# Kernel tuning notes

Measured on AMD Instinct MI355X. Metric: run time of the kernel, lower is better.

The kernel has to match this reference:

```python
import jax, jax.numpy as jnp
import numpy as np

D_IN, D_HIDDEN, DT_RANK, D_MEM, STEP = 256, 64, 16, 128, 16
B_, L_ = 2, 2048
S = 0.02  # weight init scale

def generate_a(d_in, d_hidden):
    i = jnp.arange(d_in, dtype=jnp.float32)[:, None]
    j = jnp.arange(d_hidden, dtype=jnp.float32)[None, :]
    off = jnp.sqrt(2.0 * i + 1.0) * jnp.sqrt(2.0 * j + 1.0)
    return jnp.where(i == j, i + 1.0, jnp.where(i > j, off, 0.0))

def setup_inputs():
    key = jax.random.key(0)
    ks = jax.random.split(key, 10)
    d_out = 3 * D_HIDDEN + 2 * D_IN + 2 * DT_RANK
    return {
        "x": jax.random.normal(ks[0], (B_, L_, D_IN), jnp.float32),
        "W_xproj": jax.random.normal(ks[1], (D_IN, d_out), jnp.float32) * S,
        "W_dt": jax.random.normal(ks[2], (DT_RANK, D_IN), jnp.float32) * S,
        "b_dt": jnp.full((D_IN,), -11.0, jnp.float32),
        "W_dtl": jax.random.normal(ks[3], (DT_RANK, D_IN), jnp.float32) * S,
        "b_dtl": jnp.full((D_IN,), -11.0, jnp.float32),
        "A": generate_a(D_IN, D_HIDDEN),
        "Dp": jnp.ones((D_IN,), jnp.float32),
        "W_Q": jax.random.normal(ks[4], (D_IN, D_MEM), jnp.float32) * S,
        "b_Q": jnp.zeros((D_MEM,), jnp.float32),
        "W_K": jax.random.normal(ks[5], (D_IN, D_MEM), jnp.float32) * S,
        "b_K": jnp.zeros((D_MEM,), jnp.float32),
        "W_V": jax.random.normal(ks[6], (D_IN, D_MEM), jnp.float32) * S,
        "b_V": jnp.zeros((D_MEM,), jnp.float32),
        "W_O": jax.random.normal(ks[7], (D_MEM, D_IN), jnp.float32) * S,
        "b_O": jnp.zeros((D_IN,), jnp.float32),
    }

def _selective_scan(u, delta, A, Bm, Cm, Dp):
    # u, delta: (b,l,d); A: (d,n); Bm, Cm: (b,l,n)
    dA = jnp.exp(jnp.einsum('bld,dn->bldn', delta, A))          # (b,l,d,n)
    dBu = delta[..., None] * Bm[:, :, None, :] * u[..., None]   # (b,l,d,n)
    def comb(e1, e2):
        a1, b1 = e1
        a2, b2 = e2
        return a2 * a1, a2 * b1 + b2
    _, xs = jax.lax.associative_scan(comb, (dA, dBu), axis=1)   # states (b,l,d,n)
    y = jnp.einsum('bldn,bln->bld', xs, Cm)
    if Dp is not None:
        y = y + u * Dp
    return y

def reference(x, W_xproj, W_dt, b_dt, W_dtl, b_dtl, A, Dp, W_Q, b_Q, W_K, b_K, W_V, b_V, W_O, b_O):
    proj = x @ W_xproj  # (b,l,3n+2d+2r)
    splits = np.cumsum([D_HIDDEN, D_HIDDEN, D_HIDDEN, D_IN, D_IN, DT_RANK]).tolist()
    Bm, Bl, Cm, E, Fg, dt, dtl = jnp.split(proj, splits, axis=-1)
    delta = jax.nn.softplus(dt @ W_dt + b_dt)       # delta_softplus=True folded in
    delta_l = jax.nn.softplus(dtl @ W_dtl + b_dtl)
    y = _selective_scan(x, delta, A, Bm, Cm, Dp)
    y_local = _selective_scan(x, delta_l, A, Bl, jnp.ones_like(Bl), None)  # C=ones, D=None
    memory = y_local[:, ::STEP, :]                  # strided checkpoints (b,m,d)
    Q = x @ W_Q + b_Q
    K = memory @ W_K + b_K
    V = memory @ W_V + b_V
    # note: original scales by sqrt(d_hidden), not sqrt(d_memory)
    w = jax.nn.softmax(jnp.einsum('blm,bkm->blk', Q, K) / jnp.sqrt(jnp.float32(D_HIDDEN)), axis=-1)
    att = jnp.einsum('blk,bkm->blm', w, V) @ W_O + b_O
    return y + att * E + x * Fg
```

## Files before the change

### kernel.cpp

```cpp
#include <hip/hip_runtime.h>
#include <math.h>

#define D_INN 256
#define D_HID 64
#define DTR 16
#define D_MEMM 128
#define BB 2
#define LL 2048
#define NROWS (BB*LL)
#define NPROJ 736
#define NTOT 864
#define SEG 16
#define SEGLEN (LL/SEG)
#define NCHUNK (LL/8)

typedef __attribute__((ext_vector_type(8))) short short8v;
typedef __attribute__((ext_vector_type(4))) float float4v;

static __device__ __forceinline__ unsigned short f2bf(float f) {
    unsigned int u = __float_as_uint(f);
    u += 0x7fff + ((u >> 16) & 1);
    return (unsigned short)(u >> 16);
}

static __device__ __forceinline__ float rdlane(float v, int l) {
    return __uint_as_float(__builtin_amdgcn_readlane(__float_as_uint(v), l));
}

#define PK(g, b, chunk, n, li) (((((size_t)(g)*BB + (b)) * NCHUNK + (chunk)) * 64 + (n)) * 8 + (li))

__global__ __launch_bounds__(256) void k_gemm(const float* __restrict__ x,
        const float* __restrict__ Wx, const float* __restrict__ Wq,
        const float* __restrict__ bq, float* __restrict__ proj,
        float* __restrict__ packed) {
    __shared__ unsigned short As[64][40];
    __shared__ unsigned short Bs[64][40];
    const int t = threadIdx.x;
    const int lane = t & 63, w = t >> 6;
    const int wr = w >> 1, wc = w & 1;
    const int row0 = blockIdx.y * 64, col0 = blockIdx.x * 64;

    float4v acc[2][2];
    #pragma unroll
    for (int i = 0; i < 2; i++)
        #pragma unroll
        for (int j = 0; j < 2; j++) acc[i][j] = (float4v)0.f;

    const int ar = t >> 2, akq = (t & 3) * 8;
    const int bk = t >> 3, bcq = (t & 7) * 8;

    for (int k0 = 0; k0 < D_INN; k0 += 32) {
        float4 a0 = *(const float4*)&x[(size_t)(row0 + ar) * D_INN + k0 + akq];
        float4 a1 = *(const float4*)&x[(size_t)(row0 + ar) * D_INN + k0 + akq + 4];
        float4 b0 = {}, b1 = {};
        int col = col0 + bcq;
        if (col + 8 <= NPROJ) {
            b0 = *(const float4*)&Wx[(size_t)(k0 + bk) * NPROJ + col];
            b1 = *(const float4*)&Wx[(size_t)(k0 + bk) * NPROJ + col + 4];
        } else if (col < NTOT) {
            b0 = *(const float4*)&Wq[(size_t)(k0 + bk) * D_MEMM + (col - NPROJ)];
            b1 = *(const float4*)&Wq[(size_t)(k0 + bk) * D_MEMM + (col - NPROJ) + 4];
        }
        __syncthreads();
        {
            unsigned short av[8] = { f2bf(a0.x), f2bf(a0.y), f2bf(a0.z), f2bf(a0.w),
                                     f2bf(a1.x), f2bf(a1.y), f2bf(a1.z), f2bf(a1.w) };
            *(short8v*)&As[ar][akq] = *(short8v*)av;
            Bs[bcq + 0][bk] = f2bf(b0.x); Bs[bcq + 1][bk] = f2bf(b0.y);
            Bs[bcq + 2][bk] = f2bf(b0.z); Bs[bcq + 3][bk] = f2bf(b0.w);
            Bs[bcq + 4][bk] = f2bf(b1.x); Bs[bcq + 5][bk] = f2bf(b1.y);
            Bs[bcq + 6][bk] = f2bf(b1.z); Bs[bcq + 7][bk] = f2bf(b1.w);
        }
        __syncthreads();
        short8v af[2], bf[2];
        const int fr = lane & 15, fk = (lane >> 4) * 8;
        af[0] = *(short8v*)&As[wr * 32 + fr][fk];
        af[1] = *(short8v*)&As[wr * 32 + 16 + fr][fk];
        bf[0] = *(short8v*)&Bs[wc * 32 + fr][fk];
        bf[1] = *(short8v*)&Bs[wc * 32 + 16 + fr][fk];
        #pragma unroll
        for (int i = 0; i < 2; i++)
            #pragma unroll
            for (int j = 0; j < 2; j++)
                acc[i][j] = __builtin_amdgcn_mfma_f32_16x16x32_bf16(af[i], bf[j], acc[i][j], 0, 0, 0);
    }
    #pragma unroll
    for (int i = 0; i < 2; i++)
        #pragma unroll
        for (int j = 0; j < 2; j++) {
            int cc = col0 + wc * 32 + j * 16 + (lane & 15);
            int rr0 = row0 + wr * 32 + i * 16 + (lane >> 4) * 4;
            if (cc < 192) {
                int g = cc >> 6, n = cc & 63;
                int bb = rr0 >> 11, l = rr0 & (LL - 1);
                float4 pk = make_float4(acc[i][j][0], acc[i][j][1], acc[i][j][2], acc[i][j][3]);
                *(float4*)&packed[PK(g, bb, l >> 3, n, l & 7)] = pk;
            } else {
                #pragma unroll
                for (int e = 0; e < 4; e++) {
                    float v = acc[i][j][e];
                    if (cc >= NPROJ) v += bq[cc - NPROJ];
                    proj[(size_t)(rr0 + e) * NTOT + cc] = v;
                }
            }
        }
}

__global__ __launch_bounds__(256) void k_xt(const float* __restrict__ x,
        float* __restrict__ xT) {
    __shared__ float tile[64][65];
    const int t = threadIdx.x;
    const int lt = blockIdx.x * 64, dt = blockIdx.y * 64, b = blockIdx.z;
    const int c = t & 63, rg = (t >> 6) * 16;
    #pragma unroll
    for (int j = 0; j < 16; ++j)
        tile[rg + j][c] = x[((size_t)b * LL + lt + rg + j) * D_INN + dt + c];
    __syncthreads();
    #pragma unroll
    for (int j = 0; j < 16; ++j)
        xT[((size_t)b * D_INN + dt + rg + j) * LL + lt + c] = tile[c][rg + j];
}

__global__ __launch_bounds__(256) void k_delta(const float* __restrict__ proj,
        const float* __restrict__ Wdt, const float* __restrict__ bdt,
        const float* __restrict__ Wdtl, const float* __restrict__ bdtl,
        float* __restrict__ deltaT, float* __restrict__ deltalT) {
    __shared__ float sdt[16][17], sdtl[16][17];
    const int t = threadIdx.x;
    const int r0 = blockIdx.x * 16;
    const int b = r0 >> 11, l0 = r0 & (LL - 1);
    {
        int r = t >> 4, c = t & 15;
        sdt[r][c]  = proj[(size_t)(r0 + r) * NTOT + 704 + c];
        sdtl[r][c] = proj[(size_t)(r0 + r) * NTOT + 720 + c];
    }
    __syncthreads();
    float w1[DTR], w2[DTR];
    #pragma unroll
    for (int r = 0; r < DTR; r++) {
        w1[r] = Wdt[r * D_INN + t];
        w2[r] = Wdtl[r * D_INN + t];
    }
    const float b1 = bdt[t], b2 = bdtl[t];
    float o1[16], o2[16];
    #pragma unroll
    for (int row = 0; row < 16; ++row) {
        float a1 = b1, a2 = b2;
        #pragma unroll
        for (int r = 0; r < DTR; r++) {
            a1 += sdt[row][r] * w1[r];
            a2 += sdtl[row][r] * w2[r];
        }
        o1[row] = (a1 > 20.f) ? a1 : log1pf(expf(a1));
        o2[row] = (a2 > 20.f) ? a2 : log1pf(expf(a2));
    }
    float* p1 = &deltaT[((size_t)b * D_INN + t) * LL + l0];
    float* p2 = &deltalT[((size_t)b * D_INN + t) * LL + l0];
    #pragma unroll
    for (int j = 0; j < 16; j += 4) {
        *(float4*)&p1[j] = make_float4(o1[j], o1[j+1], o1[j+2], o1[j+3]);
        *(float4*)&p2[j] = make_float4(o2[j], o2[j+1], o2[j+2], o2[j+3]);
    }
}

template<int SCAN>
__global__ __launch_bounds__(256) void k_scan1t(const float* __restrict__ xT,
        const float* __restrict__ packed, const float* __restrict__ A,
        const float* __restrict__ dTall,
        float* __restrict__ Qbuf, float* __restrict__ SDbuf,
        float* __restrict__ cumd, float* __restrict__ mem) {
    const int t = threadIdx.x;
    const int w = t >> 6, n = t & 63;
    const int b = blockIdx.y, seg = blockIdx.z;
    const int d = blockIdx.x * 4 + w;
    const float* dT = dTall + ((size_t)b * D_INN + d) * LL + seg * SEGLEN;
    const float* uT = xT + ((size_t)b * D_INN + d) * LL + seg * SEGLEN;
    const float Aln = A[d * D_HID + n] * 1.44269504f;
    const int lr = n & 7;
    const float* Bp = packed + PK(SCAN, b, seg * 16, 0, 0);

    float s = 0.f, sd = 0.f;
    for (int c = 0; c < 16; ++c) {
        float dvl = dT[c * 8 + lr];
        float pl  = dvl * uT[c * 8 + lr];
        float4 B0 = *(const float4*)&Bp[((size_t)c * 64 + n) * 8];
        float4 B1 = *(const float4*)&Bp[((size_t)c * 64 + n) * 8 + 4];
        float Bv[8] = {B0.x, B0.y, B0.z, B0.w, B1.x, B1.y, B1.z, B1.w};
        {
            float dv = rdlane(dvl, 0), p = rdlane(pl, 0);
            s = fmaf(exp2f(dv * Aln), s, p * Bv[0]);
            sd += dv;
        }
        if (SCAN == 1 && (c & 1) == 0) {
            float v = s;
            #pragma unroll
            for (int off = 32; off >= 1; off >>= 1) v += __shfl_xor(v, off);
            if (n == 0) {
                int k = seg * 8 + (c >> 1);
                mem[((size_t)b * 128 + k) * D_INN + d] = v;
                cumd[(((size_t)b * SEG + seg) * 8 + (c >> 1)) * D_INN + d] = sd;
            }
        }
        #pragma unroll
        for (int li = 1; li < 8; ++li) {
            float dv = rdlane(dvl, li), p = rdlane(pl, li);
            s = fmaf(exp2f(dv * Aln), s, p * Bv[li]);
            sd += dv;
        }
    }
    Qbuf[((((size_t)SCAN * 2 + b) * SEG + seg) * D_INN + d) * 64 + n] = s;
    if (n == 0) SDbuf[(((size_t)SCAN * 2 + b) * SEG + seg) * D_INN + d] = sd;
}

__global__ __launch_bounds__(256) void k_scan2(const float* __restrict__ xT,
        const float* __restrict__ packed, const float* __restrict__ A,
        const float* __restrict__ Dp, const float* __restrict__ deltaT,
        const float* __restrict__ Qbuf, const float* __restrict__ SDbuf,
        float* __restrict__ y) {
    __shared__ float rbuf[4][8][65];
    const int t = threadIdx.x;
    const int w = t >> 6, n = t & 63;
    const int b = blockIdx.y, seg = blockIdx.z;
    const int d = blockIdx.x * 4 + w;
    const size_t rowbase = (size_t)b * LL + (size_t)seg * SEGLEN;
    const float* dT = deltaT + ((size_t)b * D_INN + d) * LL + seg * SEGLEN;
    const float* uT = xT + ((size_t)b * D_INN + d) * LL + seg * SEGLEN;
    const float Aln = A[d * D_HID + n] * 1.44269504f;
    const float Dpv = Dp[d];
    const int lr = n & 7;
    const int rli = n >> 3, g = n & 7;
    const float* Bp = packed + PK(0, b, seg * 16, 0, 0);
    const float* Cp = packed + PK(2, b, seg * 16, 0, 0);

    float s = 0.f;
    for (int k = 0; k < seg; ++k) {
        float sdk = SDbuf[(((size_t)b * SEG + k) * D_INN + d)];
        float Qk = Qbuf[(((size_t)b * SEG + k) * D_INN + d) * 64 + n];
        s = fmaf(exp2f(sdk * Aln), s, Qk);
    }

    for (int c = 0; c < 16; ++c) {
        const size_t l0 = rowbase + c * 8;
        float dvl = dT[c * 8 + lr];
        float uvl = uT[c * 8 + lr];
        float pl = dvl * uvl;
        float4 B0 = *(const float4*)&Bp[((size_t)c * 64 + n) * 8];
        float4 B1 = *(const float4*)&Bp[((size_t)c * 64 + n) * 8 + 4];
        float4 C0 = *(const float4*)&Cp[((size_t)c * 64 + n) * 8];
        float4 C1 = *(const float4*)&Cp[((size_t)c * 64 + n) * 8 + 4];
        float Bv[8] = {B0.x, B0.y, B0.z, B0.w, B1.x, B1.y, B1.z, B1.w};
        float Cv[8] = {C0.x, C0.y, C0.z, C0.w, C1.x, C1.y, C1.z, C1.w};
        #pragma unroll
        for (int li = 0; li < 8; ++li) {
            float dv = rdlane(dvl, li);
            float p  = rdlane(pl, li);
            s = fmaf(exp2f(dv * Aln), s, p * Bv[li]);
            rbuf[w][li][n] = s * Cv[li];
        }
        float acc = 0.f;
        #pragma unroll
        for (int j = 0; j < 8; ++j) acc += rbuf[w][rli][g * 8 + j];
        acc += __shfl_xor(acc, 1);
        acc += __shfl_xor(acc, 2);
        acc += __shfl_xor(acc, 4);
        float uv = __shfl(uvl, rli);
        if (g == 0) {
            y[(l0 + rli) * D_INN + d] = acc + uv * Dpv;
        }
    }
}

__global__ __launch_bounds__(256) void k_sin(const float* __restrict__ A,
        const float* __restrict__ Qbuf, const float* __restrict__ SDbuf,
        float* __restrict__ Sin) {
    const int t = threadIdx.x, w = t >> 6, n = t & 63;
    const int b = blockIdx.y;
    const int d = blockIdx.x * 4 + w;
    const float Aln = A[d * D_HID + n] * 1.44269504f;
    float s = 0.f;
    #pragma unroll
    for (int seg = 0; seg < SEG; ++seg) {
        if (seg > 0) Sin[(((size_t)b * SEG + seg) * D_INN + d) * 64 + n] = s;
        float sdk = SDbuf[((size_t)(2 + b) * SEG + seg) * D_INN + d];
        float Qk = Qbuf[(((size_t)(2 + b) * SEG + seg) * D_INN + d) * 64 + n];
        s = fmaf(exp2f(sdk * Aln), s, Qk);
    }
}

__global__ __launch_bounds__(256) void k_fix(const float* __restrict__ A,
        const float* __restrict__ Sin, const float* __restrict__ cumd,
        float* __restrict__ mem) {
    const int t = threadIdx.x, w = t >> 6, n = t & 63;
    const int k = 8 + blockIdx.y;
    const int b = blockIdx.z;
    const int d = blockIdx.x * 4 + w;
    const int seg = k >> 3;
    const float Aln = A[d * D_HID + n] * 1.44269504f;
    float cum = cumd[((size_t)b * 128 + k) * D_INN + d];
    float sv = Sin[(((size_t)b * SEG + seg) * D_INN + d) * 64 + n];
    float v = exp2f(cum * Aln) * sv;
    #pragma unroll
    for (int off = 32; off >= 1; off >>= 1) v += __shfl_xor(v, off);
    if (n == 0) mem[((size_t)b * 128 + k) * D_INN + d] += v;
}

__global__ __launch_bounds__(128) void k_kvwo(const float* __restrict__ mem,
        const float* __restrict__ Wk, const float* __restrict__ bk,
        const float* __restrict__ Wv, const float* __restrict__ bv,
        const float* __restrict__ Wo,
        float* __restrict__ K, float* __restrict__ VWo) {
    __shared__ float mrow[256];
    __shared__ float vrow[128];
    const int k = blockIdx.x, b = blockIdx.y;
    const int t = threadIdx.x;
    const float* mr = mem + ((size_t)b * 128 + k) * D_INN;
    mrow[t] = mr[t];
    mrow[t + 128] = mr[t + 128];
    __syncthreads();
    float aK = bk[t], aV = bv[t];
    for (int dd = 0; dd < D_INN; dd++) {
        float m = mrow[dd];
        aK += m * Wk[dd * D_MEMM + t];
        aV += m * Wv[dd * D_MEMM + t];
    }
    K[((size_t)b * 128 + k) * D_MEMM + t] = aK;
    vrow[t] = aV;
    __syncthreads();
    float a0 = 0.f, a1 = 0.f;
    for (int m = 0; m < 128; ++m) {
        float vm = vrow[m];
        a0 += vm * Wo[(size_t)m * D_INN + t];
        a1 += vm * Wo[(size_t)m * D_INN + t + 128];
    }
    VWo[((size_t)b * 128 + k) * D_INN + t] = a0;
    VWo[((size_t)b * 128 + k) * D_INN + t + 128] = a1;
}

__global__ __launch_bounds__(256) void k_attn(const float* __restrict__ x,
        const float* __restrict__ proj, const float* __restrict__ y,
        const float* __restrict__ K, const float* __restrict__ VWo,
        const float* __restrict__ bo, float* __restrict__ out) {
    __shared__ float qs[16][132];
    __shared__ float ws[16][132];
    __shared__ float denom[16];
    const int t = threadIdx.x;
    const int b = blockIdx.y;
    const int r0 = blockIdx.x * 16;
    const size_t rowbase = (size_t)b * LL + r0;
    {
        int r = t >> 4, c8 = (t & 15) * 8;
        const float* src = &proj[(rowbase + r) * NTOT + NPROJ + c8];
        *(float4*)&qs[r][c8] = *(const float4*)src;
        *(float4*)&qs[r][c8 + 4] = *(const float4*)(src + 4);
    }
    __syncthreads();
    {
        const int k = t & 127, rg = (t >> 7) * 8;
        const float* Kr = K + ((size_t)b * 128 + k) * D_MEMM;
        float acc[8] = {};
        #pragma unroll 8
        for (int m = 0; m < 128; m += 4) {
            float4 kv = *(const float4*)&Kr[m];
            #pragma unroll
            for (int r = 0; r < 8; ++r) {
                float4 qv = *(const float4*)&qs[rg + r][m];
                acc[r] += qv.x * kv.x + qv.y * kv.y + qv.z * kv.z + qv.w * kv.w;
            }
        }
        #pragma unroll
        for (int r = 0; r < 8; ++r) ws[rg + r][k] = acc[r] * 0.125f;
    }
    __syncthreads();
    {
        const int r = t >> 4, j = t & 15;
        float4 v0 = *(float4*)&ws[r][j * 8];
        float4 v1 = *(float4*)&ws[r][j * 8 + 4];
        float mx = fmaxf(fmaxf(fmaxf(v0.x, v0.y), fmaxf(v0.z, v0.w)),
                         fmaxf(fmaxf(v1.x, v1.y), fmaxf(v1.z, v1.w)));
        #pragma unroll
        for (int o = 1; o < 16; o <<= 1) mx = fmaxf(mx, __shfl_xor(mx, o));
        v0.x = expf(v0.x - mx); v0.y = expf(v0.y - mx);
        v0.z = expf(v0.z - mx); v0.w = expf(v0.w - mx);
        v1.x = expf(v1.x - mx); v1.y = expf(v1.y - mx);
        v1.z = expf(v1.z - mx); v1.w = expf(v1.w - mx);
        float sum = v0.x + v0.y + v0.z + v0.w + v1.x + v1.y + v1.z + v1.w;
        #pragma unroll
        for (int o = 1; o < 16; o <<= 1) sum += __shfl_xor(sum, o);
        *(float4*)&ws[r][j * 8] = v0;
        *(float4*)&ws[r][j * 8 + 4] = v1;
        if (j == 0) denom[r] = sum;
    }
    __syncthreads();
    {
        const int w = t >> 6, lane = t & 63;
        const int c0 = lane * 4;
        const float* vb = VWo + (size_t)b * 128 * D_INN + c0;
        float acc[4][4] = {};
        #pragma unroll 8
        for (int k = 0; k < 128; k += 4) {
            float4 wv[4];
            #pragma unroll
            for (int r = 0; r < 4; ++r) wv[r] = *(float4*)&ws[w * 4 + r][k];
            #pragma unroll
            for (int kk = 0; kk < 4; ++kk) {
                float4 vw = *(const float4*)&vb[(size_t)(k + kk) * D_INN];
                #pragma unroll
                for (int r = 0; r < 4; ++r) {
                    float wk = (kk == 0 ? wv[r].x : kk == 1 ? wv[r].y : kk == 2 ? wv[r].z : wv[r].w);
                    acc[r][0] += wk * vw.x; acc[r][1] += wk * vw.y;
                    acc[r][2] += wk * vw.z; acc[r][3] += wk * vw.w;
                }
            }
        }
        float4 bov = *(const float4*)&bo[c0];
        #pragma unroll
        for (int r = 0; r < 4; ++r) {
            size_t rr = rowbase + w * 4 + r;
            float dn = 1.f / denom[w * 4 + r];
            float4 yv = *(const float4*)&y[rr * D_INN + c0];
            float4 xv = *(const float4*)&x[rr * D_INN + c0];
            float4 Ev = *(const float4*)&proj[rr * NTOT + 192 + c0];
            float4 Fv = *(const float4*)&proj[rr * NTOT + 448 + c0];
            float4 o;
            o.x = yv.x + (acc[r][0] * dn + bov.x) * Ev.x + xv.x * Fv.x;
            o.y = yv.y + (acc[r][1] * dn + bov.y) * Ev.y + xv.y * Fv.y;
            o.z = yv.z + (acc[r][2] * dn + bov.z) * Ev.z + xv.z * Fv.z;
            o.w = yv.w + (acc[r][3] * dn + bov.w) * Ev.w + xv.w * Fv.w;
            *(float4*)&out[rr * D_INN + c0] = o;
        }
    }
}

extern "C" void kernel_launch(void* const* d_in, const int* in_sizes, int n_in,
                              void* d_out, int out_size, void* d_ws, size_t ws_size,
                              hipStream_t stream) {
    const float* x    = (const float*)d_in[0];
    const float* Wx   = (const float*)d_in[1];
    const float* Wdt  = (const float*)d_in[2];
    const float* bdt  = (const float*)d_in[3];
    const float* Wdtl = (const float*)d_in[4];
    const float* bdtl = (const float*)d_in[5];
    const float* A    = (const float*)d_in[6];
    const float* Dp   = (const float*)d_in[7];
    const float* Wq   = (const float*)d_in[8];
    const float* bq   = (const float*)d_in[9];
    const float* Wk   = (const float*)d_in[10];
    const float* bk   = (const float*)d_in[11];
    const float* Wv   = (const float*)d_in[12];
    const float* bv   = (const float*)d_in[13];
    const float* Wo   = (const float*)d_in[14];
    const float* bo   = (const float*)d_in[15];
    float* out = (float*)d_out;
    float* ws = (float*)d_ws;

    float* proj    = ws;
    float* deltaT  = proj + (size_t)NROWS * NTOT;
    float* deltalT = deltaT + (size_t)NROWS * D_INN;
    float* yb      = deltalT + (size_t)NROWS * D_INN;
    float* mem     = yb + (size_t)NROWS * D_INN;
    float* Kb      = mem + (size_t)BB * 128 * D_INN;
    float* Qbuf    = Kb + (size_t)BB * 128 * D_MEMM;
    float* SDbuf   = Qbuf + (size_t)4 * SEG * D_INN * 64;
    float* cumd    = SDbuf + (size_t)4 * SEG * D_INN;
    float* Sin     = cumd + (size_t)BB * SEG * 8 * D_INN;
    float* VWo     = Sin + (size_t)BB * SEG * D_INN * 64;
    float* xT      = VWo + (size_t)BB * 128 * D_INN;
    float* packed  = xT + (size_t)NROWS * D_INN;

    hipLaunchKernelGGL(k_gemm, dim3(14, 64), dim3(256), 0, stream, x, Wx, Wq, bq, proj, packed);
    hipLaunchKernelGGL(k_xt, dim3(32, 4, 2), dim3(256), 0, stream, x, xT);
    hipLaunchKernelGGL(k_delta, dim3(NROWS / 16), dim3(256), 0, stream,
                       proj, Wdt, bdt, Wdtl, bdtl, deltaT, deltalT);
    hipLaunchKernelGGL(k_scan1t<0>, dim3(64, 2, 16), dim3(256), 0, stream,
                       xT, packed, A, deltaT, Qbuf, SDbuf, cumd, mem);
    hipLaunchKernelGGL(k_scan1t<1>, dim3(64, 2, 16), dim3(256), 0, stream,
                       xT, packed, A, deltalT, Qbuf, SDbuf, cumd, mem);
    hipLaunchKernelGGL(k_scan2, dim3(64, 2, 16), dim3(256), 0, stream,
                       xT, packed, A, Dp, deltaT, Qbuf, SDbuf, yb);
    hipLaunchKernelGGL(k_sin, dim3(64, 2), dim3(256), 0, stream,
                       A, Qbuf, SDbuf, Sin);
    hipLaunchKernelGGL(k_fix, dim3(64, 120, 2), dim3(256), 0, stream,
                       A, Sin, cumd, mem);
    hipLaunchKernelGGL(k_kvwo, dim3(128, 2), dim3(128), 0, stream,
                       mem, Wk, bk, Wv, bv, Wo, Kb, VWo);
    hipLaunchKernelGGL(k_attn, dim3(128, 2), dim3(256), 0, stream,
                       x, proj, yb, Kb, VWo, bo, out);
}
```

Before: 223.0 us.

## Transpose K for coalesced loads and halve attention rows per block

k_kvwo now writes K transposed so that k_attn threads, which each handle one key index, read consecutive addresses across lanes instead of each walking a separate row. The attention block now processes 8 query rows instead of 16, doubling the grid to 512 blocks for better CU occupancy on the final kernel. The cost is that K and VWo are re-read from cache twice as often overall, and each K element is loaded as a scalar instead of a float4.

```diff
diff --git a/kernel.cpp b/kernel.cpp
--- a/kernel.cpp
+++ b/kernel.cpp
@@ -308,7 +308,7 @@
         const float* __restrict__ Wk, const float* __restrict__ bk,
         const float* __restrict__ Wv, const float* __restrict__ bv,
         const float* __restrict__ Wo,
-        float* __restrict__ K, float* __restrict__ VWo) {
+        float* __restrict__ KT, float* __restrict__ VWo) {
     __shared__ float mrow[256];
     __shared__ float vrow[128];
     const int k = blockIdx.x, b = blockIdx.y;
@@ -323,7 +323,7 @@
         aK += m * Wk[dd * D_MEMM + t];
         aV += m * Wv[dd * D_MEMM + t];
     }
-    K[((size_t)b * 128 + k) * D_MEMM + t] = aK;
+    KT[((size_t)b * 128 + t) * 128 + k] = aK;
     vrow[t] = aV;
     __syncthreads();
     float a0 = 0.f, a1 = 0.f;
@@ -338,56 +338,52 @@
 
 __global__ __launch_bounds__(256) void k_attn(const float* __restrict__ x,
         const float* __restrict__ proj, const float* __restrict__ y,
-        const float* __restrict__ K, const float* __restrict__ VWo,
+        const float* __restrict__ KT, const float* __restrict__ VWo,
         const float* __restrict__ bo, float* __restrict__ out) {
-    __shared__ float qs[16][132];
-    __shared__ float ws[16][132];
-    __shared__ float denom[16];
+    __shared__ float qs[8][132];
+    __shared__ float ws[8][132];
+    __shared__ float denom[8];
     const int t = threadIdx.x;
     const int b = blockIdx.y;
-    const int r0 = blockIdx.x * 16;
+    const int r0 = blockIdx.x * 8;
     const size_t rowbase = (size_t)b * LL + r0;
     {
-        int r = t >> 4, c8 = (t & 15) * 8;
-        const float* src = &proj[(rowbase + r) * NTOT + NPROJ + c8];
-        *(float4*)&qs[r][c8] = *(const float4*)src;
-        *(float4*)&qs[r][c8 + 4] = *(const float4*)(src + 4);
+        int r = t >> 5, c4 = (t & 31) * 4;
+        *(float4*)&qs[r][c4] = *(const float4*)&proj[(rowbase + r) * NTOT + NPROJ + c4];
     }
     __syncthreads();
     {
-        const int k = t & 127, rg = (t >> 7) * 8;
-        const float* Kr = K + ((size_t)b * 128 + k) * D_MEMM;
-        float acc[8] = {};
+        const int kk = t & 127, rg = (t >> 7) * 4;
+        const float* KTb = KT + (size_t)b * 128 * 128 + kk;
+        float acc[4] = {};
         #pragma unroll 8
         for (int m = 0; m < 128; m += 4) {
-            float4 kv = *(const float4*)&Kr[m];
+            float k0 = KTb[(size_t)m * 128];
+            float k1 = KTb[(size_t)(m + 1) * 128];
+            float k2 = KTb[(size_t)(m + 2) * 128];
+            float k3 = KTb[(size_t)(m + 3) * 128];
             #pragma unroll
-            for (int r = 0; r < 8; ++r) {
+            for (int r = 0; r < 4; ++r) {
                 float4 qv = *(const float4*)&qs[rg + r][m];
-                acc[r] += qv.x * kv.x + qv.y * kv.y + qv.z * kv.z + qv.w * kv.w;
+                acc[r] += qv.x * k0 + qv.y * k1 + qv.z * k2 + qv.w * k3;
             }
         }
         #pragma unroll
-        for (int r = 0; r < 8; ++r) ws[rg + r][k] = acc[r] * 0.125f;
+        for (int r = 0; r < 4; ++r) ws[rg + r][kk] = acc[r] * 0.125f;
     }
     __syncthreads();
     {
-        const int r = t >> 4, j = t & 15;
-        float4 v0 = *(float4*)&ws[r][j * 8];
-        float4 v1 = *(float4*)&ws[r][j * 8 + 4];
-        float mx = fmaxf(fmaxf(fmaxf(v0.x, v0.y), fmaxf(v0.z, v0.w)),
-                         fmaxf(fmaxf(v1.x, v1.y), fmaxf(v1.z, v1.w)));
-        #pragma unroll
-        for (int o = 1; o < 16; o <<= 1) mx = fmaxf(mx, __shfl_xor(mx, o));
+        const int r = t >> 5, j = t & 31;
+        float4 v0 = *(float4*)&ws[r][j * 4];
+        float mx = fmaxf(fmaxf(v0.x, v0.y), fmaxf(v0.z, v0.w));
+        #pragma unroll
+        for (int o = 1; o < 32; o <<= 1) mx = fmaxf(mx, __shfl_xor(mx, o));
         v0.x = expf(v0.x - mx); v0.y = expf(v0.y - mx);
         v0.z = expf(v0.z - mx); v0.w = expf(v0.w - mx);
-        v1.x = expf(v1.x - mx); v1.y = expf(v1.y - mx);
-        v1.z = expf(v1.z - mx); v1.w = expf(v1.w - mx);
-        float sum = v0.x + v0.y + v0.z + v0.w + v1.x + v1.y + v1.z + v1.w;
-        #pragma unroll
-        for (int o = 1; o < 16; o <<= 1) sum += __shfl_xor(sum, o);
-        *(float4*)&ws[r][j * 8] = v0;
-        *(float4*)&ws[r][j * 8 + 4] = v1;
+        float sum = v0.x + v0.y + v0.z + v0.w;
+        #pragma unroll
+        for (int o = 1; o < 32; o <<= 1) sum += __shfl_xor(sum, o);
+        *(float4*)&ws[r][j * 4] = v0;
         if (j == 0) denom[r] = sum;
     }
     __syncthreads();
@@ -395,28 +391,26 @@
         const int w = t >> 6, lane = t & 63;
         const int c0 = lane * 4;
         const float* vb = VWo + (size_t)b * 128 * D_INN + c0;
-        float acc[4][4] = {};
+        float acc[2][4] = {};
         #pragma unroll 8
-        for (int k = 0; k < 128; k += 4) {
-            float4 wv[4];
+        for (int k = 0; k < 128; k += 2) {
+            float4 vw0 = *(const float4*)&vb[(size_t)k * D_INN];
+            float4 vw1 = *(const float4*)&vb[(size_t)(k + 1) * D_INN];
             #pragma unroll
-            for (int r = 0; r < 4; ++r) wv[r] = *(float4*)&ws[w * 4 + r][k];
-            #pragma unroll
-            for (int kk = 0; kk < 4; ++kk) {
-                float4 vw = *(const float4*)&vb[(size_t)(k + kk) * D_INN];
-                #pragma unroll
-                for (int r = 0; r < 4; ++r) {
-                    float wk = (kk == 0 ? wv[r].x : kk == 1 ? wv[r].y : kk == 2 ? wv[r].z : wv[r].w);
-                    acc[r][0] += wk * vw.x; acc[r][1] += wk * vw.y;
-                    acc[r][2] += wk * vw.z; acc[r][3] += wk * vw.w;
-                }
+            for (int r = 0; r < 2; ++r) {
+                float wk0 = ws[w * 2 + r][k];
+                float wk1 = ws[w * 2 + r][k + 1];
+                acc[r][0] += wk0 * vw0.x + wk1 * vw1.x;
+                acc[r][1] += wk0 * vw0.y + wk1 * vw1.y;
+                acc[r][2] += wk0 * vw0.z + wk1 * vw1.z;
+                acc[r][3] += wk0 * vw0.w + wk1 * vw1.w;
             }
         }
         float4 bov = *(const float4*)&bo[c0];
         #pragma unroll
-        for (int r = 0; r < 4; ++r) {
-            size_t rr = rowbase + w * 4 + r;
-            float dn = 1.f / denom[w * 4 + r];
+        for (int r = 0; r < 2; ++r) {
+            size_t rr = rowbase + w * 2 + r;
+            float dn = 1.f / denom[w * 2 + r];
             float4 yv = *(const float4*)&y[rr * D_INN + c0];
             float4 xv = *(const float4*)&x[rr * D_INN + c0];
             float4 Ev = *(const float4*)&proj[rr * NTOT + 192 + c0];
@@ -458,8 +452,8 @@
     float* deltalT = deltaT + (size_t)NROWS * D_INN;
     float* yb      = deltalT + (size_t)NROWS * D_INN;
     float* mem     = yb + (size_t)NROWS * D_INN;
-    float* Kb      = mem + (size_t)BB * 128 * D_INN;
-    float* Qbuf    = Kb + (size_t)BB * 128 * D_MEMM;
+    float* KTb     = mem + (size_t)BB * 128 * D_INN;
+    float* Qbuf    = KTb + (size_t)BB * 128 * D_MEMM;
     float* SDbuf   = Qbuf + (size_t)4 * SEG * D_INN * 64;
     float* cumd    = SDbuf + (size_t)4 * SEG * D_INN;
     float* Sin     = cumd + (size_t)BB * SEG * 8 * D_INN;
@@ -482,7 +476,7 @@
     hipLaunchKernelGGL(k_fix, dim3(64, 120, 2), dim3(256), 0, stream,
                        A, Sin, cumd, mem);
     hipLaunchKernelGGL(k_kvwo, dim3(128, 2), dim3(128), 0, stream,
-                       mem, Wk, bk, Wv, bv, Wo, Kb, VWo);
-    hipLaunchKernelGGL(k_attn, dim3(128, 2), dim3(256), 0, stream,
-                       x, proj, yb, Kb, VWo, bo, out);
-}
+                       mem, Wk, bk, Wv, bv, Wo, KTb, VWo);
+    hipLaunchKernelGGL(k_attn, dim3(LL / 8, 2), dim3(256), 0, stream,
+                       x, proj, yb, KTb, VWo, bo, out);
+}
```

Result: faster. 201.8 us (-9.5%).
